# Performance work log

Measured on AMD Instinct MI355X. Metric: run time of the kernel, lower is better.

The kernel has to match this reference:

```python
import jax, jax.numpy as jnp
import numpy as np

VOCAB, DIM, N_LORA, RANK, T, NSEG = 32000, 2048, 9, 16, 8192, 16


def setup_inputs() -> dict:
    key = jax.random.key(0)
    ks = jax.random.split(key, 7)
    input_ids = jax.random.randint(ks[0], (T,), 0, VOCAB, dtype=jnp.int32)
    weight = jax.random.normal(ks[1], (VOCAB, DIM), dtype=jnp.float32) * 0.02
    A_buffer = jax.random.normal(ks[2], (N_LORA, VOCAB, RANK), dtype=jnp.float32) * 0.02
    B_buffer = jax.random.normal(ks[3], (N_LORA, DIM, RANK), dtype=jnp.float32) * 0.02
    interior = jnp.sort(jax.random.randint(ks[4], (NSEG - 1,), 0, T, dtype=jnp.int32))
    seg_indptr = jnp.concatenate([jnp.zeros((1,), jnp.int32), interior, jnp.full((1,), T, jnp.int32)])
    weight_indices = jax.random.randint(ks[5], (NSEG,), 0, N_LORA, dtype=jnp.int32)
    scalings = jax.random.uniform(ks[6], (N_LORA,), dtype=jnp.float32, minval=0.5, maxval=2.0)
    return {"input_ids": input_ids, "weight": weight, "A_buffer": A_buffer,
            "B_buffer": B_buffer, "seg_indptr": seg_indptr,
            "weight_indices": weight_indices, "scalings": scalings}


def reference(input_ids, weight, A_buffer, B_buffer, seg_indptr, weight_indices, scalings):
    # Base embedding gather: [T, DIM]
    base = weight[input_ids]
    T_ = input_ids.shape[0]
    # Map each token to its segment, then to its per-segment LoRA slot.
    seg_id = jnp.searchsorted(seg_indptr, jnp.arange(T_, dtype=seg_indptr.dtype), side='right') - 1
    w = weight_indices[seg_id]                      # [T] lora slot per token
    active = (w != 0).astype(base.dtype)            # slot 0 == no LoRA
    # Per-token LoRA A row gather: [T, RANK]
    a = A_buffer[w, input_ids]
    a = a * (scalings[w] * active)[:, None]
    # contrib[t] = B_buffer[w[t]] @ a[t]; route via one-hot over the small
    # lora axis to avoid materializing a [T, DIM, RANK] gather of B.
    oh = jax.nn.one_hot(w, B_buffer.shape[0], dtype=base.dtype)  # [T, L]
    contrib = jnp.einsum('tl,tr,ldr->td', oh, a, B_buffer)
    return base + contrib
```

## Files before the change

### kernel.cpp

```cpp
#include <hip/hip_runtime.h>

#define VOCAB 32000
#define DIM 2048
#define N_LORA 9
#define RANK 16
#define NSEG 16
#define TB 32
#define BLOCK 256

__global__ __launch_bounds__(BLOCK) void lora_embed_kernel(
    const int* __restrict__ input_ids,
    const float* __restrict__ weight,
    const float* __restrict__ A_buffer,
    const float* __restrict__ B_buffer,
    const int* __restrict__ seg_indptr,
    const int* __restrict__ weight_indices,
    const float* __restrict__ scalings,
    float* __restrict__ out,
    int T)
{
    __shared__ int ids_s[TB];
    __shared__ int w_s[TB];
    __shared__ float scale_s[TB];
    __shared__ float4 a_s[TB][RANK / 4];

    const int tid = threadIdx.x;
    const int t0 = blockIdx.x * TB;

    if (tid < TB) {
        int tg = t0 + tid;
        int tc = tg < T ? tg : T - 1;
        int id = input_ids[tc];
        int seg = -1;
        #pragma unroll
        for (int i = 0; i < NSEG; ++i)
            seg += (seg_indptr[i] <= tc) ? 1 : 0;
        int w = weight_indices[seg];
        ids_s[tid] = id;
        w_s[tid] = w;
        scale_s[tid] = (w != 0) ? scalings[w] : 0.0f;
    }
    __syncthreads();

    if (tid < TB * 4) {
        const int t = tid >> 2, q = tid & 3;
        const float4* arow = reinterpret_cast<const float4*>(
            A_buffer + ((size_t)w_s[t] * VOCAB + (size_t)ids_s[t]) * RANK);
        float4 av = arow[q];
        const float s = scale_s[t];
        av.x *= s; av.y *= s; av.z *= s; av.w *= s;
        a_s[t][q] = av;
    }
    __syncthreads();

    const int d = (blockIdx.y * BLOCK + tid) * 4;

    float4 b[16];
    int wcur = -1;

    #pragma unroll 4
    for (int t = 0; t < TB; ++t) {
        const int tg = t0 + t;
        if (tg >= T) break;

        const int w = w_s[t];
        if (w != wcur) {
            wcur = w;
            const float4* bp = reinterpret_cast<const float4*>(
                B_buffer + ((size_t)w * DIM + (size_t)d) * RANK);
            #pragma unroll
            for (int j = 0; j < 16; ++j) b[j] = bp[j];
        }

        const float4 a0 = a_s[t][0], a1 = a_s[t][1], a2 = a_s[t][2], a3 = a_s[t][3];

        float4 acc;
        acc.x = b[ 0].x*a0.x + b[ 0].y*a0.y + b[ 0].z*a0.z + b[ 0].w*a0.w
              + b[ 1].x*a1.x + b[ 1].y*a1.y + b[ 1].z*a1.z + b[ 1].w*a1.w
              + b[ 2].x*a2.x + b[ 2].y*a2.y + b[ 2].z*a2.z + b[ 2].w*a2.w
              + b[ 3].x*a3.x + b[ 3].y*a3.y + b[ 3].z*a3.z + b[ 3].w*a3.w;
        acc.y = b[ 4].x*a0.x + b[ 4].y*a0.y + b[ 4].z*a0.z + b[ 4].w*a0.w
              + b[ 5].x*a1.x + b[ 5].y*a1.y + b[ 5].z*a1.z + b[ 5].w*a1.w
              + b[ 6].x*a2.x + b[ 6].y*a2.y + b[ 6].z*a2.z + b[ 6].w*a2.w
              + b[ 7].x*a3.x + b[ 7].y*a3.y + b[ 7].z*a3.z + b[ 7].w*a3.w;
        acc.z = b[ 8].x*a0.x + b[ 8].y*a0.y + b[ 8].z*a0.z + b[ 8].w*a0.w
              + b[ 9].x*a1.x + b[ 9].y*a1.y + b[ 9].z*a1.z + b[ 9].w*a1.w
              + b[10].x*a2.x + b[10].y*a2.y + b[10].z*a2.z + b[10].w*a2.w
              + b[11].x*a3.x + b[11].y*a3.y + b[11].z*a3.z + b[11].w*a3.w;
        acc.w = b[12].x*a0.x + b[12].y*a0.y + b[12].z*a0.z + b[12].w*a0.w
              + b[13].x*a1.x + b[13].y*a1.y + b[13].z*a1.z + b[13].w*a1.w
              + b[14].x*a2.x + b[14].y*a2.y + b[14].z*a2.z + b[14].w*a2.w
              + b[15].x*a3.x + b[15].y*a3.y + b[15].z*a3.z + b[15].w*a3.w;

        const float4 wv = *reinterpret_cast<const float4*>(
            weight + (size_t)ids_s[t] * DIM + d);

        float4 o;
        o.x = wv.x + acc.x; o.y = wv.y + acc.y;
        o.z = wv.z + acc.z; o.w = wv.w + acc.w;
        *reinterpret_cast<float4*>(out + (size_t)tg * DIM + d) = o;
    }
}

extern "C" void kernel_launch(void* const* d_in, const int* in_sizes, int n_in,
                              void* d_out, int out_size, void* d_ws, size_t ws_size,
                              hipStream_t stream) {
    const int*   input_ids      = (const int*)d_in[0];
    const float* weight         = (const float*)d_in[1];
    const float* A_buffer       = (const float*)d_in[2];
    const float* B_buffer       = (const float*)d_in[3];
    const int*   seg_indptr     = (const int*)d_in[4];
    const int*   weight_indices = (const int*)d_in[5];
    const float* scalings       = (const float*)d_in[6];
    float* out = (float*)d_out;

    const int T = in_sizes[0];
    dim3 grid((T + TB - 1) / TB, DIM / (BLOCK * 4));
    lora_embed_kernel<<<grid, BLOCK, 0, stream>>>(
        input_ids, weight, A_buffer, B_buffer,
        seg_indptr, weight_indices, scalings, out, T);
}
```

Baseline: 33.47 us.

## Halve token tile, use nontemporal output stores, and split full/tail token loops

Reduces tokens per block from 32 to 16, doubling the grid size for more parallelism. Output writes become nontemporal stores so the streamed result bypasses cache retention. The token loop is split into a bounds-check-free fast path for full tiles and a separate tail loop. The base embedding value is folded into the dot-product sum. Smaller tiles mean more redundant prologue work (segment search, A gather) and more B reloads per block.

```diff
diff --git a/kernel.cpp b/kernel.cpp
--- a/kernel.cpp
+++ b/kernel.cpp
@@ -5,8 +5,61 @@
 #define N_LORA 9
 #define RANK 16
 #define NSEG 16
-#define TB 32
+#define TB 16
 #define BLOCK 256
+
+typedef float f32x4 __attribute__((ext_vector_type(4)));
+
+struct Smem {
+    int ids[TB];
+    int w[TB];
+    float scale[TB];
+    f32x4 a[TB][RANK / 4];
+};
+
+__device__ __forceinline__ void token_body(
+    int tk, int t0, int d,
+    const Smem& s,
+    const float* __restrict__ weight,
+    const float* __restrict__ B_buffer,
+    float* __restrict__ out,
+    f32x4 (&b)[16], int& wcur)
+{
+    const int w = s.w[tk];
+    if (w != wcur) {
+        wcur = w;
+        const f32x4* bp = reinterpret_cast<const f32x4*>(
+            B_buffer + ((size_t)w * DIM + (size_t)d) * RANK);
+        #pragma unroll
+        for (int j = 0; j < 16; ++j) b[j] = bp[j];
+    }
+    const f32x4 a0 = s.a[tk][0], a1 = s.a[tk][1], a2 = s.a[tk][2], a3 = s.a[tk][3];
+    const f32x4 wv = *reinterpret_cast<const f32x4*>(
+        weight + (size_t)s.ids[tk] * DIM + d);
+    f32x4 o;
+    o.x = wv.x
+        + b[ 0].x*a0.x + b[ 0].y*a0.y + b[ 0].z*a0.z + b[ 0].w*a0.w
+        + b[ 1].x*a1.x + b[ 1].y*a1.y + b[ 1].z*a1.z + b[ 1].w*a1.w
+        + b[ 2].x*a2.x + b[ 2].y*a2.y + b[ 2].z*a2.z + b[ 2].w*a2.w
+        + b[ 3].x*a3.x + b[ 3].y*a3.y + b[ 3].z*a3.z + b[ 3].w*a3.w;
+    o.y = wv.y
+        + b[ 4].x*a0.x + b[ 4].y*a0.y + b[ 4].z*a0.z + b[ 4].w*a0.w
+        + b[ 5].x*a1.x + b[ 5].y*a1.y + b[ 5].z*a1.z + b[ 5].w*a1.w
+        + b[ 6].x*a2.x + b[ 6].y*a2.y + b[ 6].z*a2.z + b[ 6].w*a2.w
+        + b[ 7].x*a3.x + b[ 7].y*a3.y + b[ 7].z*a3.z + b[ 7].w*a3.w;
+    o.z = wv.z
+        + b[ 8].x*a0.x + b[ 8].y*a0.y + b[ 8].z*a0.z + b[ 8].w*a0.w
+        + b[ 9].x*a1.x + b[ 9].y*a1.y + b[ 9].z*a1.z + b[ 9].w*a1.w
+        + b[10].x*a2.x + b[10].y*a2.y + b[10].z*a2.z + b[10].w*a2.w
+        + b[11].x*a3.x + b[11].y*a3.y + b[11].z*a3.z + b[11].w*a3.w;
+    o.w = wv.w
+        + b[12].x*a0.x + b[12].y*a0.y + b[12].z*a0.z + b[12].w*a0.w
+        + b[13].x*a1.x + b[13].y*a1.y + b[13].z*a1.z + b[13].w*a1.w
+        + b[14].x*a2.x + b[14].y*a2.y + b[14].z*a2.z + b[14].w*a2.w
+        + b[15].x*a3.x + b[15].y*a3.y + b[15].z*a3.z + b[15].w*a3.w;
+    __builtin_nontemporal_store(o, reinterpret_cast<f32x4*>(
+        out + (size_t)(t0 + tk) * DIM + d));
+}
 
 __global__ __launch_bounds__(BLOCK) void lora_embed_kernel(
     const int* __restrict__ input_ids,
@@ -19,10 +72,7 @@
     float* __restrict__ out,
     int T)
 {
-    __shared__ int ids_s[TB];
-    __shared__ int w_s[TB];
-    __shared__ float scale_s[TB];
-    __shared__ float4 a_s[TB][RANK / 4];
+    __shared__ Smem s;
 
     const int tid = threadIdx.x;
     const int t0 = blockIdx.x * TB;
@@ -36,69 +86,34 @@
         for (int i = 0; i < NSEG; ++i)
             seg += (seg_indptr[i] <= tc) ? 1 : 0;
         int w = weight_indices[seg];
-        ids_s[tid] = id;
-        w_s[tid] = w;
-        scale_s[tid] = (w != 0) ? scalings[w] : 0.0f;
+        s.ids[tid] = id;
+        s.w[tid] = w;
+        s.scale[tid] = (w != 0) ? scalings[w] : 0.0f;
     }
     __syncthreads();
 
     if (tid < TB * 4) {
         const int t = tid >> 2, q = tid & 3;
-        const float4* arow = reinterpret_cast<const float4*>(
-            A_buffer + ((size_t)w_s[t] * VOCAB + (size_t)ids_s[t]) * RANK);
-        float4 av = arow[q];
-        const float s = scale_s[t];
-        av.x *= s; av.y *= s; av.z *= s; av.w *= s;
-        a_s[t][q] = av;
+        const f32x4* arow = reinterpret_cast<const f32x4*>(
+            A_buffer + ((size_t)s.w[t] * VOCAB + (size_t)s.ids[t]) * RANK);
+        f32x4 av = arow[q];
+        s.a[t][q] = av * s.scale[t];
     }
     __syncthreads();
 
     const int d = (blockIdx.y * BLOCK + tid) * 4;
 
-    float4 b[16];
+    f32x4 b[16];
     int wcur = -1;
 
-    #pragma unroll 4
-    for (int t = 0; t < TB; ++t) {
-        const int tg = t0 + t;
-        if (tg >= T) break;
-
-        const int w = w_s[t];
-        if (w != wcur) {
-            wcur = w;
-            const float4* bp = reinterpret_cast<const float4*>(
-                B_buffer + ((size_t)w * DIM + (size_t)d) * RANK);
-            #pragma unroll
-            for (int j = 0; j < 16; ++j) b[j] = bp[j];
-        }
-
-        const float4 a0 = a_s[t][0], a1 = a_s[t][1], a2 = a_s[t][2], a3 = a_s[t][3];
-
-        float4 acc;
-        acc.x = b[ 0].x*a0.x + b[ 0].y*a0.y + b[ 0].z*a0.z + b[ 0].w*a0.w
-              + b[ 1].x*a1.x + b[ 1].y*a1.y + b[ 1].z*a1.z + b[ 1].w*a1.w
-              + b[ 2].x*a2.x + b[ 2].y*a2.y + b[ 2].z*a2.z + b[ 2].w*a2.w
-              + b[ 3].x*a3.x + b[ 3].y*a3.y + b[ 3].z*a3.z + b[ 3].w*a3.w;
-        acc.y = b[ 4].x*a0.x + b[ 4].y*a0.y + b[ 4].z*a0.z + b[ 4].w*a0.w
-              + b[ 5].x*a1.x + b[ 5].y*a1.y + b[ 5].z*a1.z + b[ 5].w*a1.w
-              + b[ 6].x*a2.x + b[ 6].y*a2.y + b[ 6].z*a2.z + b[ 6].w*a2.w
-              + b[ 7].x*a3.x + b[ 7].y*a3.y + b[ 7].z*a3.z + b[ 7].w*a3.w;
-        acc.z = b[ 8].x*a0.x + b[ 8].y*a0.y + b[ 8].z*a0.z + b[ 8].w*a0.w
-              + b[ 9].x*a1.x + b[ 9].y*a1.y + b[ 9].z*a1.z + b[ 9].w*a1.w
-              + b[10].x*a2.x + b[10].y*a2.y + b[10].z*a2.z + b[10].w*a2.w
-              + b[11].x*a3.x + b[11].y*a3.y + b[11].z*a3.z + b[11].w*a3.w;
-        acc.w = b[12].x*a0.x + b[12].y*a0.y + b[12].z*a0.z + b[12].w*a0.w
-              + b[13].x*a1.x + b[13].y*a1.y + b[13].z*a1.z + b[13].w*a1.w
-              + b[14].x*a2.x + b[14].y*a2.y + b[14].z*a2.z + b[14].w*a2.w
-              + b[15].x*a3.x + b[15].y*a3.y + b[15].z*a3.z + b[15].w*a3.w;
-
-        const float4 wv = *reinterpret_cast<const float4*>(
-            weight + (size_t)ids_s[t] * DIM + d);
-
-        float4 o;
-        o.x = wv.x + acc.x; o.y = wv.y + acc.y;
-        o.z = wv.z + acc.z; o.w = wv.w + acc.w;
-        *reinterpret_cast<float4*>(out + (size_t)tg * DIM + d) = o;
+    if (t0 + TB <= T) {
+        #pragma unroll 4
+        for (int t = 0; t < TB; ++t)
+            token_body(t, t0, d, s, weight, B_buffer, out, b, wcur);
+    } else {
+        const int nt = T - t0;
+        for (int t = 0; t < nt; ++t)
+            token_body(t, t0, d, s, weight, B_buffer, out, b, wcur);
     }
 }
 
```

New measurement: 36.95 us. +10.4%, slower.
